# Optimization experiments

Hardware: AMD Instinct MI355X
Metric: run time of the kernel (lower is better)

The kernel has to match this reference:

```python
import jax, jax.numpy as jnp
import numpy as np

UP = 4
INTERVAL = 4      # coarse base interval from init
SAMP_INT = 4      # sampling_interval (fine, diagonal region)
DWID = 2          # diagonal_width
K = 3             # sample_size (AutoSample conv kernel)
Q2 = float(2 ** (INTERVAL + 2)); L2 = 2 ** (8 - INTERVAL - 2) + 1   # coarse full-space LUT: 64, 5
Q1 = float(2 ** SAMP_INT);       L1 = 2 ** (8 - SAMP_INT) + 1       # fine diagonal LUT: 16, 17
DW = 2 * DWID + 1
R1 = L1 * DW * DW * DW


def round_ste(v):
    # straight-through round, as in MuLUT's round_func
    return v + jax.lax.stop_gradient(jnp.round(v) - v)


def _msb_lsb(v, q, L):
    i = jnp.clip(jnp.floor(v / q).astype(jnp.int32), 0, L - 2)
    return i, v - i.astype(v.dtype) * q


def _simplex(f, q):
    # 4D simplex (tetrahedral) interpolation weights + vertex increments.
    # f: [..., 4] LSB fractions. Sorting descending reproduces the 24-case if/else.
    order = jnp.argsort(-f, axis=-1)
    fs = jnp.take_along_axis(f, order, axis=-1)
    w = jnp.stack([q - fs[..., 0],
                   fs[..., 0] - fs[..., 1],
                   fs[..., 1] - fs[..., 2],
                   fs[..., 2] - fs[..., 3],
                   fs[..., 3]], axis=-1) / q              # [...,5]
    oh = jax.nn.one_hot(order, 4, dtype=jnp.int32)        # [...,4,4]
    inc = jnp.cumsum(oh, axis=-2)
    inc = jnp.concatenate([jnp.zeros_like(inc[..., :1, :]), inc], axis=-2)  # [...,5,4]
    return w, inc


def _interp_mode(img, sw, w1, w2, res, r2i):
    # img [N,1,H,W] in [0,255]; sw [4,1,K,K]; w1 [R1,oc] fine LUT; w2 [L2^4,oc] coarse LUT; res [oc]
    pad = K - 1
    imgp = jnp.pad(img, ((0, 0), (0, 0), (0, pad), (0, pad)), mode='edge')
    abcd = jax.lax.conv_general_dilated(imgp, sw, (1, 1), 'VALID',
                                        dimension_numbers=('NCHW', 'OIHW', 'NCHW'))
    v = jnp.clip(jnp.moveaxis(abcd, 1, -1), 0.0, 255.0)   # [N,H,W,4] sampled (a,b,c,d)
    # coarse full-space path (compress2)
    i2, f2 = _msb_lsb(v, Q2, L2)
    wgt2, inc2 = _simplex(f2, Q2)
    vert2 = jnp.clip(i2[..., None, :] + inc2, 0, L2 - 1)  # [N,H,W,5,4]
    flat2 = ((vert2[..., 0] * L2 + vert2[..., 1]) * L2 + vert2[..., 2]) * L2 + vert2[..., 3]
    out2 = jnp.einsum('...v,...vo->...o', wgt2, w2[flat2])
    # fine diagonal path (compress1 via ref2index)
    i1, f1 = _msb_lsb(v, Q1, L1)
    wgt1, inc1 = _simplex(f1, Q1)
    vert1 = jnp.clip(i1[..., None, :] + inc1, 0, L1 - 1)
    jx = vert1[..., 0]
    off = jnp.clip(vert1[..., 1:] - jx[..., None] + DWID, 0, DW - 1)
    rows = r2i[jx, off[..., 0], off[..., 1], off[..., 2]]
    out1 = jnp.einsum('...v,...vo->...o', wgt1, w1[rows])
    within = ((jnp.abs(i1[..., 1] - i1[..., 0]) <= DWID - 1) &
              (jnp.abs(i1[..., 2] - i1[..., 0]) <= DWID - 1) &
              (jnp.abs(i1[..., 3] - i1[..., 0]) <= DWID - 1))
    return jnp.where(within[..., None], out1, out2) + res  # [N,H,W,oc]


def _stage(img, sw, w1, w2, res, r2i):
    # mode x rotation ensemble; sw [M,4,1,K,K]; w1 [M,R1,oc]; w2 [M,625,oc]; res [M,oc]
    M = sw.shape[0]
    acc = 0.0
    for m in range(M):
        for r in range(4):
            xr = jnp.rot90(img, r, axes=(2, 3))
            o = _interp_mode(xr, sw[m], w1[m], w2[m], res[m], r2i)
            o = jnp.moveaxis(o, -1, 1)                    # [N,oc,h,w]
            acc = acc + jnp.rot90(o, -r, axes=(2, 3))
    return acc / (4.0 * M)


def _stage6(feat, sw, w1, w2, res, r2i):
    # feat [N,4,H,W]; sw [M,4,4,1,K,K]; w1 [M,4,R1,up^2]; res [M,4,up^2]
    M = sw.shape[0]
    acc = 0.0
    for m in range(M):
        for c in range(4):
            for r in range(4):
                xr = jnp.rot90(feat[:, c:c + 1], r, axes=(2, 3))
                o = _interp_mode(xr, sw[m, c], w1[m, c], w2[m, c], res[m, c], r2i)
                N, h, w, _ = o.shape
                # pixel shuffle before rotating back
                o = o.reshape(N, h, w, UP, UP).transpose(0, 1, 3, 2, 4).reshape(N, 1, h * UP, w * UP)
                acc = acc + jnp.rot90(o, -r, axes=(2, 3))
    return acc / (4.0 * 4.0 * M)


def setup_inputs() -> dict:
    key = jax.random.key(0)
    ks = jax.random.split(key, 14)
    B, H, W = 2, 192, 192
    x = jax.random.uniform(ks[0], (B, 1, H, W), jnp.float32)
    ref2index = jnp.arange(R1, dtype=jnp.int64).reshape(L1, DW, DW, DW)
    # samplers scaled to keep sampled pixel values roughly in [0,255]
    samp_s123 = jax.random.uniform(ks[1], (3, 3, 4, 1, K, K), jnp.float32) / (K * K)
    samp_s4 = jax.random.uniform(ks[2], (3, 4, 1, K, K), jnp.float32) / (K * K)
    samp_s6 = jax.random.uniform(ks[3], (3, 4, 4, 1, K, K), jnp.float32) / (K * K)
    w1_s123 = jax.random.normal(ks[4], (3, 3, R1, 2), jnp.float32) * 0.1
    w2_s123 = jax.random.normal(ks[5], (3, 3, L2 ** 4, 2), jnp.float32) * 0.1
    res_s123 = jax.random.normal(ks[6], (3, 3, 2), jnp.float32) * 0.01
    w1_s4 = jax.random.normal(ks[7], (3, R1, 1), jnp.float32) * 0.1
    w2_s4 = jax.random.normal(ks[8], (3, L2 ** 4, 1), jnp.float32) * 0.1
    res_s4 = jax.random.normal(ks[9], (3, 1), jnp.float32) * 0.01
    w1_s6 = jax.random.normal(ks[10], (3, 4, R1, UP * UP), jnp.float32) * 0.1
    w2_s6 = jax.random.normal(ks[11], (3, 4, L2 ** 4, UP * UP), jnp.float32) * 0.1
    res_s6 = jax.random.normal(ks[12], (3, 4, UP * UP), jnp.float32) * 0.01
    return {'x': x, 'ref2index': ref2index,
            'samp_s123': samp_s123, 'w1_s123': w1_s123, 'w2_s123': w2_s123, 'res_s123': res_s123,
            'samp_s4': samp_s4, 'w1_s4': w1_s4, 'w2_s4': w2_s4, 'res_s4': res_s4,
            'samp_s6': samp_s6, 'w1_s6': w1_s6, 'w2_s6': w2_s6, 'res_s6': res_s6}


def reference(x, ref2index, samp_s123, w1_s123, w2_s123, res_s123,
              samp_s4, w1_s4, w2_s4, res_s4,
              samp_s6, w1_s6, w2_s6, res_s6):
    cur = round_ste(jnp.clip(x * 255.0, 0.0, 255.0))
    refine = []
    for s in range(3):  # stages 1-3, out_c=2: ch0 -> refine, ch1 -> next stage
        pred = _stage(cur, samp_s123[s], w1_s123[s], w2_s123[s], res_s123[s], ref2index)
        y = round_ste(jnp.clip(pred * 255.0, 0.0, 255.0))
        refine.append(y[:, 0:1])
        cur = y[:, 1:2]
    pred = _stage(cur, samp_s4, w1_s4, w2_s4, res_s4, ref2index)  # stage 4, out_c=1
    refine.append(round_ste(jnp.clip(pred * 255.0, 0.0, 255.0)))
    feat = jnp.concatenate(refine, axis=1)  # [B,4,H,W]
    hr = _stage6(feat, samp_s6, w1_s6, w2_s6, res_s6, ref2index)  # [B,1,H*up,W*up]
    return jnp.clip(hr * 255.0, 0.0, 255.0) / 255.0
```

## Files before the change

kernel.cpp:

```cpp
#include <hip/hip_runtime.h>

#define HW   192
#define HW2  (HW*HW)
#define NPIX (2*HW2)
#define NUP  (HW*4)

__device__ __forceinline__ float clamp255f(float v){ return fminf(fmaxf(v,0.f),255.f); }

__device__ __forceinline__ void simplex_core(const float v4[4],
    bool& within_o, int idx[5], float wgt[5])
{
  float f1[4], f2[4]; int i1[4], i2[4];
#pragma unroll
  for (int k=0;k<4;k++){
    float vk = clamp255f(v4[k]);
    int a = (int)(vk*0.0625f);   a = a>15?15:a;
    int b = (int)(vk*0.015625f); b = b>3 ?3 :b;
    i1[k]=a; f1[k]=vk-(float)a*16.f;
    i2[k]=b; f2[k]=vk-(float)b*64.f;
  }
  const int d1=i1[1]-i1[0], d2=i1[2]-i1[0], d3=i1[3]-i1[0];
  const bool within = (d1<=1)&&(d1>=-1)&&(d2<=1)&&(d2>=-1)&&(d3<=1)&&(d3>=-1);
  within_o = within;

  float ff[4]; int ii[4];
#pragma unroll
  for (int k=0;k<4;k++){ ff[k]= within?f1[k]:f2[k]; ii[k]= within?i1[k]:i2[k]; }
  const float Q    = within?16.f:64.f;
  const float qinv = within?0.0625f:0.015625f;

  const int rk0 = (ff[1]> ff[0]) + (ff[2]> ff[0]) + (ff[3]> ff[0]);
  const int rk1 = (ff[0]>=ff[1]) + (ff[2]> ff[1]) + (ff[3]> ff[1]);
  const int rk2 = (ff[0]>=ff[2]) + (ff[1]>=ff[2]) + (ff[3]> ff[2]);
  const int rk3 = (ff[0]>=ff[3]) + (ff[1]>=ff[3]) + (ff[2]>=ff[3]);

  float a0=ff[0],a1=ff[1],a2=ff[2],a3=ff[3],t;
  t=fmaxf(a0,a1); a1=fminf(a0,a1); a0=t;
  t=fmaxf(a2,a3); a3=fminf(a2,a3); a2=t;
  t=fmaxf(a0,a2); a2=fminf(a0,a2); a0=t;
  t=fmaxf(a1,a3); a3=fminf(a1,a3); a1=t;
  t=fmaxf(a1,a2); a2=fminf(a1,a2); a1=t;

  wgt[0]=(Q-a0)*qinv; wgt[1]=(a0-a1)*qinv; wgt[2]=(a1-a2)*qinv;
  wgt[3]=(a2-a3)*qinv; wgt[4]=a3*qinv;

#pragma unroll
  for (int t5=0;t5<5;t5++){
    const int c0 = rk0<t5, c1 = rk1<t5, c2 = rk2<t5, c3 = rk3<t5;
    const int A0 = ii[0]+c0;
    const int A1 = within ? (d1 + c1 - c0 + 2) : (ii[1]+c1);
    const int A2 = within ? (d2 + c2 - c0 + 2) : (ii[2]+c2);
    const int A3 = within ? (d3 + c3 - c0 + 2) : (ii[3]+c3);
    idx[t5] = A0*125 + A1*25 + A2*5 + A3;
  }
}

__device__ __forceinline__ void interp_accum16(const float v4[4],
    const float* __restrict__ w1m, const float* __restrict__ w2m, float acc[16])
{
  bool within; int idx[5]; float wgt[5];
  simplex_core(v4, within, idx, wgt);
  const float* tab = within ? w1m : w2m;
#pragma unroll
  for (int t5=0;t5<5;t5++){
    const float w = wgt[t5];
    const float4* row = reinterpret_cast<const float4*>(tab + (size_t)idx[t5]*16);
    float4 p0=row[0], p1=row[1], p2=row[2], p3=row[3];
    acc[0]=fmaf(w,p0.x,acc[0]); acc[1]=fmaf(w,p0.y,acc[1]); acc[2]=fmaf(w,p0.z,acc[2]); acc[3]=fmaf(w,p0.w,acc[3]);
    acc[4]=fmaf(w,p1.x,acc[4]); acc[5]=fmaf(w,p1.y,acc[5]); acc[6]=fmaf(w,p1.z,acc[6]); acc[7]=fmaf(w,p1.w,acc[7]);
    acc[8]=fmaf(w,p2.x,acc[8]); acc[9]=fmaf(w,p2.y,acc[9]); acc[10]=fmaf(w,p2.z,acc[10]); acc[11]=fmaf(w,p2.w,acc[11]);
    acc[12]=fmaf(w,p3.x,acc[12]); acc[13]=fmaf(w,p3.y,acc[13]); acc[14]=fmaf(w,p3.z,acc[14]); acc[15]=fmaf(w,p3.w,acc[15]);
  }
}

template<int OUTC, bool QUANT>
__global__ void __launch_bounds__(512) stage_kernel(
    const float* __restrict__ img, const float* __restrict__ sw,
    const float* __restrict__ w1,  const float* __restrict__ w2,
    const float* __restrict__ res, float* __restrict__ outA, float* __restrict__ outB)
{
  __shared__ __align__(16) float lds_w1[3*2125*OUTC];
  for (int i = threadIdx.x; i < 3*2125*OUTC; i += 512) lds_w1[i] = w1[i];
  __syncthreads();

  const int t   = blockIdx.x*512 + threadIdx.x;
  const int r   = t & 3;
  const int pix = t >> 2;
  const int b = pix/HW2, rem = pix - b*HW2;
  const int y = rem/HW,  x   = rem - y*HW;
  const float* im = img + b*HW2;

  float tap[9];
#pragma unroll
  for (int kh=0;kh<3;kh++)
#pragma unroll
    for (int kw=0;kw<3;kw++){
      int ry = (r==0)? y+kh : (r==1)? y+kw : (r==2)? y-kh : y-kw;
      int cx = (r==0)? x+kw : (r==1)? x-kh : (r==2)? x-kw : x+kh;
      ry = min(max(ry,0),HW-1); cx = min(max(cx,0),HW-1);
      float p = im[ry*HW+cx];
      if constexpr (QUANT) p = rintf(clamp255f(p*255.f));
      tap[kh*3+kw]=p;
    }

  float pm[3][OUTC];
#pragma unroll
  for (int m=0;m<3;m++){
    const float* swm = sw + m*36;
    float v[4];
#pragma unroll
    for (int oc=0;oc<4;oc++){
      float a=0.f;
#pragma unroll
      for (int k=0;k<9;k++) a = fmaf(swm[oc*9+k], tap[k], a);
      v[oc]=a;
    }

    bool within; int idx[5]; float wgt[5];
    simplex_core(v, within, idx, wgt);

    float s[OUTC];
#pragma unroll
    for (int c=0;c<OUTC;c++) s[c]=0.f;
    if constexpr (OUTC==2){
      const float2* l2 = reinterpret_cast<const float2*>(lds_w1) + m*2125;
      const float2* g2 = reinterpret_cast<const float2*>(w2) + m*625;
      if (within){
#pragma unroll
        for (int t5=0;t5<5;t5++){
          const float2 p = l2[idx[t5]];
          s[0]=fmaf(wgt[t5],p.x,s[0]); s[1]=fmaf(wgt[t5],p.y,s[1]);
        }
      } else {
#pragma unroll
        for (int t5=0;t5<5;t5++){
          const float2 p = g2[idx[t5]];
          s[0]=fmaf(wgt[t5],p.x,s[0]); s[1]=fmaf(wgt[t5],p.y,s[1]);
        }
      }
    } else {
      const float* l1 = lds_w1 + m*2125;
      const float* g1 = w2 + m*625;
      if (within){
#pragma unroll
        for (int t5=0;t5<5;t5++) s[0]=fmaf(wgt[t5], l1[idx[t5]], s[0]);
      } else {
#pragma unroll
        for (int t5=0;t5<5;t5++) s[0]=fmaf(wgt[t5], g1[idx[t5]], s[0]);
      }
    }
#pragma unroll
    for (int c=0;c<OUTC;c++) pm[m][c] = s[c] + res[m*OUTC+c];
  }

  const int lane = threadIdx.x & 63;
  const int base = lane & ~3;
  float acc[OUTC];
#pragma unroll
  for (int c=0;c<OUTC;c++) acc[c]=0.f;
#pragma unroll
  for (int m=0;m<3;m++)
#pragma unroll
    for (int rr=0;rr<4;rr++){
#pragma unroll
      for (int c=0;c<OUTC;c++) acc[c] += __shfl(pm[m][c], base+rr, 64);
    }

  if (r==0){
    outA[pix] = rintf(clamp255f((acc[0]/12.0f)*255.0f));
    if constexpr (OUTC==2)
      outB[pix] = rintf(clamp255f((acc[1]/12.0f)*255.0f));
  }
}

__global__ void __launch_bounds__(256) stage6_kernel(
    const float* __restrict__ feat, const float* __restrict__ sw,
    const float* __restrict__ w1,   const float* __restrict__ w2,
    const float* __restrict__ res,  float* __restrict__ out)
{
  __shared__ float lds[4][64][17];
  const int lane = threadIdx.x & 63;
  const int c    = threadIdx.x >> 6;
  const int r    = lane & 3;
  const int pl   = lane >> 2;
  const int pix  = blockIdx.x*16 + pl;
  const int b  = pix/HW2, rem = pix - b*HW2;
  const int by = rem/HW,  bx  = rem - by*HW;

  const float* im = feat + (size_t)c*NPIX + b*HW2;
  float tap[9];
#pragma unroll
  for (int kh=0;kh<3;kh++)
#pragma unroll
    for (int kw=0;kw<3;kw++){
      int ry = (r==0)? by+kh : (r==1)? by+kw : (r==2)? by-kh : by-kw;
      int cx = (r==0)? bx+kw : (r==1)? bx-kh : (r==2)? bx-kw : bx+kh;
      ry = min(max(ry,0),HW-1); cx = min(max(cx,0),HW-1);
      tap[kh*3+kw] = im[ry*HW+cx];
    }

  float racc[16];
#pragma unroll
  for (int i=0;i<16;i++) racc[i]=0.f;

#pragma unroll
  for (int m=0;m<3;m++){
    const int mc = m*4 + c;
    const float* swmc = sw + mc*36;
    float v[4];
#pragma unroll
    for (int oc=0;oc<4;oc++){
      float a=0.f;
#pragma unroll
      for (int k=0;k<9;k++) a = fmaf(swmc[oc*9+k], tap[k], a);
      v[oc]=a;
    }
    const float* remc = res + mc*16;
#pragma unroll
    for (int i=0;i<16;i++) racc[i] += remc[i];
    interp_accum16(v, w1 + (size_t)mc*2125*16, w2 + (size_t)mc*625*16, racc);
  }

#pragma unroll
  for (int i=0;i<16;i++) lds[c][lane][i] = racc[i];
  __syncthreads();

  if (c == 0){
    float s[16];
#pragma unroll
    for (int i=0;i<16;i++)
      s[i] = ((lds[0][lane][i] + lds[1][lane][i]) + lds[2][lane][i]) + lds[3][lane][i];

    float po[16];
    if (r==0){
#pragma unroll
      for (int i=0;i<16;i++) po[i]=s[i];
    } else if (r==1){
#pragma unroll
      for (int p=0;p<4;p++)
#pragma unroll
        for (int q=0;q<4;q++) po[p*4+q]=s[(3-q)*4+p];
    } else if (r==2){
#pragma unroll
      for (int p=0;p<4;p++)
#pragma unroll
        for (int q=0;q<4;q++) po[p*4+q]=s[(3-p)*4+(3-q)];
    } else {
#pragma unroll
      for (int p=0;p<4;p++)
#pragma unroll
        for (int q=0;q<4;q++) po[p*4+q]=s[q*4+(3-p)];
    }

#pragma unroll
    for (int i=0;i<16;i++){
      po[i] += __shfl_xor(po[i],1);
      po[i] += __shfl_xor(po[i],2);
    }

    auto fin = [](float sv)->float{
      const float hr = sv/48.0f;
      return fminf(fmaxf(hr*255.f,0.f),255.f)/255.f;
    };
    float* op = out + (size_t)b*(NUP*NUP) + (size_t)(4*by+r)*NUP + 4*bx;
    *reinterpret_cast<float4*>(op) =
        make_float4(fin(po[r*4+0]),fin(po[r*4+1]),fin(po[r*4+2]),fin(po[r*4+3]));
  }
}

extern "C" void kernel_launch(void* const* d_in, const int* in_sizes, int n_in,
                              void* d_out, int out_size, void* d_ws, size_t ws_size,
                              hipStream_t stream)
{
  const float* x       = (const float*)d_in[0];
  const float* samp123 = (const float*)d_in[2];
  const float* w1123   = (const float*)d_in[3];
  const float* w2123   = (const float*)d_in[4];
  const float* res123  = (const float*)d_in[5];
  const float* samp4   = (const float*)d_in[6];
  const float* w14     = (const float*)d_in[7];
  const float* w24     = (const float*)d_in[8];
  const float* res4    = (const float*)d_in[9];
  const float* samp6   = (const float*)d_in[10];
  const float* w16     = (const float*)d_in[11];
  const float* w26     = (const float*)d_in[12];
  const float* res6    = (const float*)d_in[13];

  float* ws   = (float*)d_ws;
  float* feat = ws;
  float* curA = ws + 4*NPIX;
  float* curB = ws + 5*NPIX;

  const int GS = NPIX*4/512;
  const int G6 = NPIX/16;

  stage_kernel<2,true ><<<GS,512,0,stream>>>(x,    samp123,      w1123,        w2123,       res123,    feat,        curB);
  stage_kernel<2,false><<<GS,512,0,stream>>>(curB, samp123+108,  w1123+12750,  w2123+3750,  res123+6,  feat+NPIX,   curA);
  stage_kernel<2,false><<<GS,512,0,stream>>>(curA, samp123+216,  w1123+25500,  w2123+7500,  res123+12, feat+2*NPIX, curB);
  stage_kernel<1,false><<<GS,512,0,stream>>>(curB, samp4,        w14,          w24,         res4,      feat+3*NPIX, nullptr);
  stage6_kernel<<<G6,256,0,stream>>>(feat, samp6, w16, w26, res6, (float*)d_out);
}
```

Baseline: 194.3 us.

## Split stage kernel modes across warps and drop LDS LUT staging

Restructures the stage kernels so each 192-thread block handles 16 pixels, with each of the three wavefronts computing one mode (rotation group) instead of one thread looping over all three modes. The per-block copy of the fine LUT into shared memory is removed, and LUT lookups now read from global memory through the cache. Partial results are reduced through a small shared array after a barrier. This is meant to remove the large per-block LDS fill and raise occupancy, at the cost of uncached global gathers for the fine LUT and an extra sync plus reduction by only one wavefront.

```diff
diff --git a/kernel.cpp b/kernel.cpp
--- a/kernel.cpp
+++ b/kernel.cpp
@@ -74,18 +74,17 @@
 }
 
 template<int OUTC, bool QUANT>
-__global__ void __launch_bounds__(512) stage_kernel(
+__global__ void __launch_bounds__(192) stage_kernel(
     const float* __restrict__ img, const float* __restrict__ sw,
     const float* __restrict__ w1,  const float* __restrict__ w2,
     const float* __restrict__ res, float* __restrict__ outA, float* __restrict__ outB)
 {
-  __shared__ __align__(16) float lds_w1[3*2125*OUTC];
-  for (int i = threadIdx.x; i < 3*2125*OUTC; i += 512) lds_w1[i] = w1[i];
-  __syncthreads();
-
-  const int t   = blockIdx.x*512 + threadIdx.x;
-  const int r   = t & 3;
-  const int pix = t >> 2;
+  __shared__ float red[3][64][3];
+  const int lane = threadIdx.x & 63;
+  const int m    = threadIdx.x >> 6;
+  const int r    = lane & 3;
+  const int pl   = lane >> 2;
+  const int pix  = blockIdx.x*16 + pl;
   const int b = pix/HW2, rem = pix - b*HW2;
   const int y = rem/HW,  x   = rem - y*HW;
   const float* im = img + b*HW2;
@@ -103,73 +102,58 @@
       tap[kh*3+kw]=p;
     }
 
-  float pm[3][OUTC];
-#pragma unroll
-  for (int m=0;m<3;m++){
-    const float* swm = sw + m*36;
-    float v[4];
-#pragma unroll
-    for (int oc=0;oc<4;oc++){
-      float a=0.f;
-#pragma unroll
-      for (int k=0;k<9;k++) a = fmaf(swm[oc*9+k], tap[k], a);
-      v[oc]=a;
-    }
-
-    bool within; int idx[5]; float wgt[5];
-    simplex_core(v, within, idx, wgt);
-
-    float s[OUTC];
-#pragma unroll
-    for (int c=0;c<OUTC;c++) s[c]=0.f;
-    if constexpr (OUTC==2){
-      const float2* l2 = reinterpret_cast<const float2*>(lds_w1) + m*2125;
-      const float2* g2 = reinterpret_cast<const float2*>(w2) + m*625;
-      if (within){
-#pragma unroll
-        for (int t5=0;t5<5;t5++){
-          const float2 p = l2[idx[t5]];
-          s[0]=fmaf(wgt[t5],p.x,s[0]); s[1]=fmaf(wgt[t5],p.y,s[1]);
-        }
-      } else {
-#pragma unroll
-        for (int t5=0;t5<5;t5++){
-          const float2 p = g2[idx[t5]];
-          s[0]=fmaf(wgt[t5],p.x,s[0]); s[1]=fmaf(wgt[t5],p.y,s[1]);
-        }
+  const float* swm = sw + m*36;
+  float v[4];
+#pragma unroll
+  for (int oc=0;oc<4;oc++){
+    float a=0.f;
+#pragma unroll
+    for (int k=0;k<9;k++) a = fmaf(swm[oc*9+k], tap[k], a);
+    v[oc]=a;
+  }
+
+  bool within; int idx[5]; float wgt[5];
+  simplex_core(v, within, idx, wgt);
+
+  float s[OUTC];
+#pragma unroll
+  for (int c=0;c<OUTC;c++) s[c]=0.f;
+  if constexpr (OUTC==2){
+    const float2* tab = within
+        ? reinterpret_cast<const float2*>(w1) + m*2125
+        : reinterpret_cast<const float2*>(w2) + m*625;
+#pragma unroll
+    for (int t5=0;t5<5;t5++){
+      const float2 p = tab[idx[t5]];
+      s[0]=fmaf(wgt[t5],p.x,s[0]); s[1]=fmaf(wgt[t5],p.y,s[1]);
+    }
+  } else {
+    const float* tab = within ? (w1 + m*2125) : (w2 + m*625);
+#pragma unroll
+    for (int t5=0;t5<5;t5++) s[0]=fmaf(wgt[t5], tab[idx[t5]], s[0]);
+  }
+
+#pragma unroll
+  for (int c=0;c<OUTC;c++) red[m][lane][c] = s[c] + res[m*OUTC+c];
+  __syncthreads();
+
+  if (threadIdx.x < 64){
+    const int base = lane & ~3;
+    float acc[OUTC];
+#pragma unroll
+    for (int c=0;c<OUTC;c++) acc[c]=0.f;
+#pragma unroll
+    for (int mm=0;mm<3;mm++)
+#pragma unroll
+      for (int rr=0;rr<4;rr++){
+#pragma unroll
+        for (int c=0;c<OUTC;c++) acc[c] += red[mm][base+rr][c];
       }
-    } else {
-      const float* l1 = lds_w1 + m*2125;
-      const float* g1 = w2 + m*625;
-      if (within){
-#pragma unroll
-        for (int t5=0;t5<5;t5++) s[0]=fmaf(wgt[t5], l1[idx[t5]], s[0]);
-      } else {
-#pragma unroll
-        for (int t5=0;t5<5;t5++) s[0]=fmaf(wgt[t5], g1[idx[t5]], s[0]);
-      }
-    }
-#pragma unroll
-    for (int c=0;c<OUTC;c++) pm[m][c] = s[c] + res[m*OUTC+c];
-  }
-
-  const int lane = threadIdx.x & 63;
-  const int base = lane & ~3;
-  float acc[OUTC];
-#pragma unroll
-  for (int c=0;c<OUTC;c++) acc[c]=0.f;
-#pragma unroll
-  for (int m=0;m<3;m++)
-#pragma unroll
-    for (int rr=0;rr<4;rr++){
-#pragma unroll
-      for (int c=0;c<OUTC;c++) acc[c] += __shfl(pm[m][c], base+rr, 64);
-    }
-
-  if (r==0){
-    outA[pix] = rintf(clamp255f((acc[0]/12.0f)*255.0f));
-    if constexpr (OUTC==2)
-      outB[pix] = rintf(clamp255f((acc[1]/12.0f)*255.0f));
+    if (r==0){
+      outA[pix] = rintf(clamp255f((acc[0]/12.0f)*255.0f));
+      if constexpr (OUTC==2)
+        outB[pix] = rintf(clamp255f((acc[1]/12.0f)*255.0f));
+    }
   }
 }
 
@@ -291,12 +275,12 @@
   float* curA = ws + 4*NPIX;
   float* curB = ws + 5*NPIX;
 
-  const int GS = NPIX*4/512;
+  const int GS = NPIX/16;
   const int G6 = NPIX/16;
 
-  stage_kernel<2,true ><<<GS,512,0,stream>>>(x,    samp123,      w1123,        w2123,       res123,    feat,        curB);
-  stage_kernel<2,false><<<GS,512,0,stream>>>(curB, samp123+108,  w1123+12750,  w2123+3750,  res123+6,  feat+NPIX,   curA);
-  stage_kernel<2,false><<<GS,512,0,stream>>>(curA, samp123+216,  w1123+25500,  w2123+7500,  res123+12, feat+2*NPIX, curB);
-  stage_kernel<1,false><<<GS,512,0,stream>>>(curB, samp4,        w14,          w24,         res4,      feat+3*NPIX, nullptr);
+  stage_kernel<2,true ><<<GS,192,0,stream>>>(x,    samp123,      w1123,        w2123,       res123,    feat,        curB);
+  stage_kernel<2,false><<<GS,192,0,stream>>>(curB, samp123+108,  w1123+12750,  w2123+3750,  res123+6,  feat+NPIX,   curA);
+  stage_kernel<2,false><<<GS,192,0,stream>>>(curA, samp123+216,  w1123+25500,  w2123+7500,  res123+12, feat+2*NPIX, curB);
+  stage_kernel<1,false><<<GS,192,0,stream>>>(curB, samp4,        w14,          w24,         res4,      feat+3*NPIX, nullptr);
   stage6_kernel<<<G6,256,0,stream>>>(feat, samp6, w16, w26, res6, (float*)d_out);
 }
```

Result: no change. 192.6 us (-0.9%).
